# Kernel optimization log

Measured on AMD Instinct MI355X. Metric: run time of the kernel, lower is better.

## Reference

```python
import math
import jax, jax.numpy as jnp
import numpy as np

EMBED = 1024
INTERNAL = 1024  # EMBED // downsample_rate(=1)
HEADS = 16


def setup_inputs() -> dict:
    key = jax.random.key(0)
    ks = jax.random.split(key, 11)
    b, n, m = 2, 2048, 2048
    s = 1.0 / math.sqrt(EMBED)
    inp = {
        "q": jax.random.normal(ks[0], (b, n, EMBED), jnp.float32),
        "k": jax.random.normal(ks[1], (b, m, EMBED), jnp.float32),
        "v": jax.random.normal(ks[2], (b, m, EMBED), jnp.float32),
        # Linear params (torch Linear: y = x @ W.T + b); store as [in, out].
        "Wq": jax.random.normal(ks[3], (EMBED, INTERNAL), jnp.float32) * s,
        "bq": jax.random.normal(ks[4], (INTERNAL,), jnp.float32) * s,
        "Wk": jax.random.normal(ks[5], (EMBED, INTERNAL), jnp.float32) * s,
        "bk": jax.random.normal(ks[6], (INTERNAL,), jnp.float32) * s,
        "Wv": jax.random.normal(ks[7], (EMBED, INTERNAL), jnp.float32) * s,
        "bv": jax.random.normal(ks[8], (INTERNAL,), jnp.float32) * s,
        "Wo": jax.random.normal(ks[9], (INTERNAL, EMBED), jnp.float32) * s,
        "bo": jax.random.normal(ks[10], (EMBED,), jnp.float32) * s,
    }
    return inp


def _split_heads(x):  # [b, n, c] -> [b, h, n, c/h]
    b, n, c = x.shape
    return x.reshape(b, n, HEADS, c // HEADS).transpose(0, 2, 1, 3)


def reference(q, k, v, Wq, bq, Wk, bk, Wv, bv, Wo, bo):
    qh = _split_heads(q @ Wq + bq)
    kh = _split_heads(k @ Wk + bk)
    vh = _split_heads(v @ Wv + bv)
    c_per_head = kh.shape[-1]
    attn = jnp.einsum("bhnc,bhmc->bhnm", qh, kh) / math.sqrt(c_per_head)
    attn = jax.nn.softmax(attn, axis=-1)
    out = jnp.einsum("bhnm,bhmc->bhnc", attn, vh)
    b, h, n, ch = out.shape
    out = out.transpose(0, 2, 1, 3).reshape(b, n, h * ch)
    return out @ Wo + bo
```

## Files before the change

kernel.cpp:

```cpp
#include <hip/hip_runtime.h>

#define EMBED 1024
#define HEADS 16
#define DHEAD 64
#define BATCH 2
#define SEQ 2048
#define ROWS (BATCH*SEQ)
#define SZA (ROWS*EMBED)
#define SW (EMBED*EMBED)

typedef _Float16 f16;
typedef __attribute__((ext_vector_type(2))) __fp16 h16x2;
typedef __attribute__((ext_vector_type(4))) _Float16 f16x4;
typedef __attribute__((ext_vector_type(8))) _Float16 f16x8;
typedef __attribute__((ext_vector_type(4))) float f32x4;

__device__ __forceinline__ void gld16(const f16* g, f16* lds) {
  __builtin_amdgcn_global_load_lds(
      (const __attribute__((address_space(1))) void*)g,
      (__attribute__((address_space(3))) void*)lds, 16, 0, 0);
}

__global__ __launch_bounds__(256) void pre_kernel(
    const float* __restrict__ q, const float* __restrict__ k,
    const float* __restrict__ v, f16* __restrict__ qc,
    f16* __restrict__ kc, f16* __restrict__ vc,
    const float* __restrict__ w0, const float* __restrict__ w1,
    const float* __restrict__ w2, const float* __restrict__ w3,
    f16* __restrict__ o0, f16* __restrict__ o1,
    f16* __restrict__ o2, f16* __restrict__ o3) {
  __shared__ float tile[32][33];
  const int y = blockIdx.y;
  if (y < 3) {
    const float* in = y == 0 ? q : y == 1 ? k : v;
    f16* out       = y == 0 ? qc : y == 1 ? kc : vc;
    int i = blockIdx.x * 256 + threadIdx.x;
    float4 f = ((const float4* __restrict__)in)[i];
    union { f16 h[4]; short4 s4; } u;
    u.h[0] = (f16)f.x; u.h[1] = (f16)f.y; u.h[2] = (f16)f.z; u.h[3] = (f16)f.w;
    ((short4* __restrict__)out)[i] = u.s4;
    return;
  }
  const int x = blockIdx.x;
  const int z = x >> 10, by = (x >> 5) & 31, bx = x & 31;
  const float* in = z == 0 ? w0 : z == 1 ? w1 : z == 2 ? w2 : w3;
  f16* out       = z == 0 ? o0 : z == 1 ? o1 : z == 2 ? o2 : o3;
  int tx = threadIdx.x & 31, ty = threadIdx.x >> 5;
  #pragma unroll
  for (int i = 0; i < 32; i += 8)
    tile[ty + i][tx] = in[(by*32 + ty + i)*EMBED + bx*32 + tx];
  __syncthreads();
  #pragma unroll
  for (int i = 0; i < 32; i += 8)
    out[(bx*32 + ty + i)*EMBED + by*32 + tx] = (f16)tile[tx][ty + i];
}

__global__ __launch_bounds__(256) void gemm3_kernel(
    const f16* __restrict__ qc, const f16* __restrict__ kc, const f16* __restrict__ vc,
    const f16* __restrict__ Wqt, const f16* __restrict__ Wkt, const f16* __restrict__ Wvt,
    const float* __restrict__ bq, const float* __restrict__ bk, const float* __restrict__ bv,
    f16* __restrict__ Qp, f16* __restrict__ Kp, f16* __restrict__ Vtg) {
  __shared__ __align__(16) f16 As[128*32];
  __shared__ __align__(16) f16 Bs[128*32];
  const int z = blockIdx.y;
  const f16 *A, *Bt; const float* bias; f16* C;
  int mbase, nbase, N, biasrow;
  if (z == 0)      { A=qc;  Bt=Wqt; bias=bq; C=Qp;  mbase=(blockIdx.x&31)*128; nbase=(blockIdx.x>>5)*128; N=EMBED; biasrow=0; }
  else if (z == 1) { A=kc;  Bt=Wkt; bias=bk; C=Kp;  mbase=(blockIdx.x&31)*128; nbase=(blockIdx.x>>5)*128; N=EMBED; biasrow=0; }
  else             { A=Wvt; Bt=vc;  bias=bv; C=Vtg; mbase=(blockIdx.x&7)*128;  nbase=(blockIdx.x>>3)*128; N=ROWS;  biasrow=1; }
  const int K = EMBED;
  const int tid = threadIdx.x;
  const int wave = tid >> 6, lane = tid & 63;
  const int lg = lane >> 4, lr = lane & 15;
  const int wm = (wave >> 1) * 64, wn = (wave & 1) * 64;
  const int sr = lane >> 2, sc = (lane & 3) * 8;
  const f16* gA0 = A  + (size_t)(mbase + wave*16 + sr)*K + sc;
  const f16* gA1 = A  + (size_t)(mbase + 64 + wave*16 + sr)*K + sc;
  const f16* gB0 = Bt + (size_t)(nbase + wave*16 + sr)*K + sc;
  const f16* gB1 = Bt + (size_t)(nbase + 64 + wave*16 + sr)*K + sc;
  f16* lA0 = &As[(wave*16)*32];
  f16* lA1 = &As[(64 + wave*16)*32];
  f16* lB0 = &Bs[(wave*16)*32];
  f16* lB1 = &Bs[(64 + wave*16)*32];
  f32x4 acc[4][4] = {};
  for (int k0 = 0; k0 < K; k0 += 32) {
    __syncthreads();
    gld16(gA0 + k0, lA0);
    gld16(gA1 + k0, lA1);
    gld16(gB0 + k0, lB0);
    gld16(gB1 + k0, lB1);
    __syncthreads();
    f16x8 af[4], bf[4];
    #pragma unroll
    for (int mt = 0; mt < 4; mt++)
      af[mt] = *(const f16x8*)&As[(wm + mt*16 + lr)*32 + lg*8];
    #pragma unroll
    for (int nt = 0; nt < 4; nt++)
      bf[nt] = *(const f16x8*)&Bs[(wn + nt*16 + lr)*32 + lg*8];
    #pragma unroll
    for (int mt = 0; mt < 4; mt++)
      #pragma unroll
      for (int nt = 0; nt < 4; nt++)
        acc[mt][nt] = __builtin_amdgcn_mfma_f32_16x16x32_f16(af[mt], bf[nt], acc[mt][nt], 0, 0, 0);
  }
  #pragma unroll
  for (int mt = 0; mt < 4; mt++)
    #pragma unroll
    for (int nt = 0; nt < 4; nt++)
      #pragma unroll
      for (int i = 0; i < 4; i++) {
        int row = mbase + wm + mt*16 + lg*4 + i;
        int col = nbase + wn + nt*16 + lr;
        float val = acc[mt][nt][i] + (biasrow ? bias[row] : bias[col]);
        C[(size_t)row*N + col] = (f16)val;
      }
}

__global__ __launch_bounds__(256) void gemmo_kernel(
    const f16* __restrict__ A, const f16* __restrict__ Bt,
    const float* __restrict__ bias, float* __restrict__ Cf) {
  __shared__ __align__(16) f16 As[128*32];
  __shared__ __align__(16) f16 Bs[64*32];
  const int K = EMBED, N = EMBED;
  const int tid = threadIdx.x;
  const int wave = tid >> 6, lane = tid & 63;
  const int lg = lane >> 4, lr = lane & 15;
  const int mbase = blockIdx.x * 128, nbase = blockIdx.y * 64;
  const int wm = (wave >> 1) * 64, wn = (wave & 1) * 32;
  const int sr = wave*16 + (lane >> 2), sc = (lane & 3) * 8;
  const f16* gA0 = A  + (size_t)(mbase + sr)*K + sc;
  const f16* gA1 = A  + (size_t)(mbase + 64 + sr)*K + sc;
  const f16* gB  = Bt + (size_t)(nbase + sr)*K + sc;
  f16* lA0 = &As[(wave*16)*32];
  f16* lA1 = &As[(64 + wave*16)*32];
  f16* lB  = &Bs[(wave*16)*32];
  f32x4 acc[4][2] = {};
  for (int k0 = 0; k0 < K; k0 += 32) {
    __syncthreads();
    gld16(gA0 + k0, lA0);
    gld16(gA1 + k0, lA1);
    gld16(gB  + k0, lB);
    __syncthreads();
    f16x8 af[4], bf[2];
    #pragma unroll
    for (int mt = 0; mt < 4; mt++)
      af[mt] = *(const f16x8*)&As[(wm + mt*16 + lr)*32 + lg*8];
    #pragma unroll
    for (int nt = 0; nt < 2; nt++)
      bf[nt] = *(const f16x8*)&Bs[(wn + nt*16 + lr)*32 + lg*8];
    #pragma unroll
    for (int mt = 0; mt < 4; mt++)
      #pragma unroll
      for (int nt = 0; nt < 2; nt++)
        acc[mt][nt] = __builtin_amdgcn_mfma_f32_16x16x32_f16(af[mt], bf[nt], acc[mt][nt], 0, 0, 0);
  }
  #pragma unroll
  for (int mt = 0; mt < 4; mt++)
    #pragma unroll
    for (int nt = 0; nt < 2; nt++)
      #pragma unroll
      for (int i = 0; i < 4; i++) {
        int row = mbase + wm + mt*16 + lg*4 + i;
        int col = nbase + wn + nt*16 + lr;
        Cf[(size_t)row*N + col] = acc[mt][nt][i] + bias[col];
      }
}

__global__ __launch_bounds__(256, 2) void attn_kernel(
    const f16* __restrict__ Qp, const f16* __restrict__ Kp,
    const f16* __restrict__ Vt, f16* __restrict__ Ob) {
  __shared__ __align__(16) f16 Ks[4096];
  __shared__ __align__(16) f16 Vs[4096];
  const int tid = threadIdx.x;
  const int wave = tid >> 6, lane = tid & 63;
  const int lg = lane >> 4, lr = lane & 15;
  const int gid = blockIdx.x;
  const int bh  = (gid & 7)*4 + ((gid >> 3) & 3);
  const int qblk = gid >> 5;
  const int h = bh & 15, b = bh >> 4;
  const int q0 = qblk*128 + wave*32;
  const f16* Qh = Qp + (size_t)b*SEQ*EMBED + h*DHEAD;
  const f16* Kh = Kp + (size_t)b*SEQ*EMBED + h*DHEAD;
  const f16* Vh = Vt + (size_t)h*DHEAD*ROWS + (size_t)b*SEQ;

  const f16* kst[2]; const f16* vst[2]; f16* kdst[2]; f16* vdst[2];
  #pragma unroll
  for (int m = 0; m < 2; m++) {
    int sgrp = m*4 + wave;
    int srow = sgrp*8 + (lane >> 3);
    int sch  = (lane & 7) ^ (srow & 7);
    int prow = ((srow>>5)&1)*32 + ((srow>>4)&1)*4 + ((srow>>2)&3)*8 + (srow&3);
    kst[m] = Kh + (size_t)prow*EMBED + sch*8;
    vst[m] = Vh + (size_t)srow*ROWS + sch*8;
    kdst[m] = &Ks[sgrp*512];
    vdst[m] = &Vs[sgrp*512];
  }

  f16x8 qf[2][2];
  #pragma unroll
  for (int qb = 0; qb < 2; qb++)
    #pragma unroll
    for (int ds = 0; ds < 2; ds++)
      qf[qb][ds] = *(const f16x8*)&Qh[(size_t)(q0 + qb*16 + lr)*EMBED + ds*32 + lg*8];

  const int c0 = ((lg)     ^ (lr & 7)) * 8;
  const int c1 = ((4 + lg) ^ (lr & 7)) * 8;

  f32x4 o[4][2] = {};
  float ls[2] = {};
  const float SC = 0.18033688011f;

  for (int kt = 0; kt < SEQ; kt += 64) {
    __syncthreads();
    gld16(kst[0] + (size_t)kt*EMBED, kdst[0]);
    gld16(kst[1] + (size_t)kt*EMBED, kdst[1]);
    gld16(vst[0] + kt, vdst[0]);
    gld16(vst[1] + kt, vdst[1]);
    __syncthreads();

    f16x8 ka[4][2];
    #pragma unroll
    for (int nb = 0; nb < 4; nb++) {
      ka[nb][0] = *(const f16x8*)&Ks[(nb*16 + lr)*64 + c0];
      ka[nb][1] = *(const f16x8*)&Ks[(nb*16 + lr)*64 + c1];
    }
    f32x4 sa[2][4];
    #pragma unroll
    for (int nb = 0; nb < 4; nb++)
      #pragma unroll
      for (int qb = 0; qb < 2; qb++) {
        f32x4 z = {0.f, 0.f, 0.f, 0.f};
        z = __builtin_amdgcn_mfma_f32_16x16x32_f16(ka[nb][0], qf[qb][0], z, 0, 0, 0);
        z = __builtin_amdgcn_mfma_f32_16x16x32_f16(ka[nb][1], qf[qb][1], z, 0, 0, 0);
        sa[qb][nb] = z;
      }

    f16x8 va[4][2];
    #pragma unroll
    for (int dm = 0; dm < 4; dm++) {
      va[dm][0] = *(const f16x8*)&Vs[(dm*16 + lr)*64 + c0];
      va[dm][1] = *(const f16x8*)&Vs[(dm*16 + lr)*64 + c1];
    }

    f16x8 pf[2][2];
    #pragma unroll
    for (int qb = 0; qb < 2; qb++) {
      float p[4][4];
      #pragma unroll
      for (int nb = 0; nb < 4; nb++)
        #pragma unroll
        for (int i = 0; i < 4; i++) {
          p[nb][i] = __builtin_amdgcn_exp2f(sa[qb][nb][i]*SC - 8.0f);
          ls[qb] += p[nb][i];
        }
      union { f16x8 v; h16x2 h2[4]; } u0, u1;
      u0.h2[0] = __builtin_amdgcn_cvt_pkrtz(p[0][0], p[0][1]);
      u0.h2[1] = __builtin_amdgcn_cvt_pkrtz(p[0][2], p[0][3]);
      u0.h2[2] = __builtin_amdgcn_cvt_pkrtz(p[1][0], p[1][1]);
      u0.h2[3] = __builtin_amdgcn_cvt_pkrtz(p[1][2], p[1][3]);
      u1.h2[0] = __builtin_amdgcn_cvt_pkrtz(p[2][0], p[2][1]);
      u1.h2[1] = __builtin_amdgcn_cvt_pkrtz(p[2][2], p[2][3]);
      u1.h2[2] = __builtin_amdgcn_cvt_pkrtz(p[3][0], p[3][1]);
      u1.h2[3] = __builtin_amdgcn_cvt_pkrtz(p[3][2], p[3][3]);
      pf[qb][0] = u0.v;
      pf[qb][1] = u1.v;
    }

    #pragma unroll
    for (int ks = 0; ks < 2; ks++)
      #pragma unroll
      for (int qb = 0; qb < 2; qb++)
        #pragma unroll
        for (int dm = 0; dm < 4; dm++)
          o[dm][qb] = __builtin_amdgcn_mfma_f32_16x16x32_f16(va[dm][ks], pf[qb][ks], o[dm][qb], 0, 0, 0);
  }

  float inv[2];
  #pragma unroll
  for (int qb = 0; qb < 2; qb++) {
    float s = ls[qb];
    s += __shfl_xor(s, 16);
    s += __shfl_xor(s, 32);
    inv[qb] = 1.f / s;
  }

  #pragma unroll
  for (int qb = 0; qb < 2; qb++) {
    const size_t rowb = (size_t)(b*SEQ + q0 + qb*16 + lr)*EMBED + h*DHEAD;
    #pragma unroll
    for (int dm = 0; dm < 4; dm++) {
      f16x4 w;
      #pragma unroll
      for (int i = 0; i < 4; i++) w[i] = (f16)(o[dm][qb][i] * inv[qb]);
      *(f16x4*)&Ob[rowb + dm*16 + 4*lg] = w;
    }
  }
}

extern "C" void kernel_launch(void* const* d_in, const int* in_sizes, int n_in,
                              void* d_out, int out_size, void* d_ws, size_t ws_size,
                              hipStream_t stream) {
  (void)in_sizes; (void)n_in; (void)out_size; (void)ws_size;
  const float* q  = (const float*)d_in[0];
  const float* k  = (const float*)d_in[1];
  const float* v  = (const float*)d_in[2];
  const float* Wq = (const float*)d_in[3];
  const float* bq = (const float*)d_in[4];
  const float* Wk = (const float*)d_in[5];
  const float* bk = (const float*)d_in[6];
  const float* Wv = (const float*)d_in[7];
  const float* bv = (const float*)d_in[8];
  const float* Wo = (const float*)d_in[9];
  const float* bo = (const float*)d_in[10];
  float* out = (float*)d_out;

  f16* w   = (f16*)d_ws;
  f16* qc  = w;
  f16* kc  = qc + SZA;
  f16* vc  = kc + SZA;
  f16* Qp  = vc + SZA;
  f16* Kp  = Qp + SZA;
  f16* Vtg = Kp + SZA;
  f16* Ob  = Vtg + SZA;
  f16* Wqt = Ob + SZA;
  f16* Wkt = Wqt + SW;
  f16* Wvt = Wkt + SW;
  f16* Wot = Wvt + SW;

  dim3 pg(4096, 4);
  pre_kernel<<<pg, 256, 0, stream>>>(q, k, v, qc, kc, vc,
                                     Wq, Wk, Wv, Wo, Wqt, Wkt, Wvt, Wot);
  dim3 g3(256, 3);
  gemm3_kernel<<<g3, 256, 0, stream>>>(qc, kc, vc, Wqt, Wkt, Wvt, bq, bk, bv, Qp, Kp, Vtg);
  attn_kernel<<<512, 256, 0, stream>>>(Qp, Kp, Vtg, Ob);
  dim3 go(ROWS/128, EMBED/64);
  gemmo_kernel<<<go, 256, 0, stream>>>(Ob, Wot, bo, out);
}
```

Baseline: 216.4 us.

## Double-buffer K/V tiles and fold softmax scale and row sums into MFMA

The attention loop now uses double-buffered LDS for K and V. The next tile's global-to-LDS loads are issued before computing on the current tile, and only one barrier remains per iteration. The softmax scale is applied in the Q projection epilogue (z==0), and the -8 offset becomes the MFMA accumulator init, which removes per-element FMAs. Row sums are computed by an extra MFMA against a ones vector instead of scalar adds and shuffles. s_setprio brackets are added around the MFMA sections. LDS use doubles, which may reduce occupancy, and the extra MFMAs add matrix-core work.

```diff
diff --git a/kernel.cpp b/kernel.cpp
--- a/kernel.cpp
+++ b/kernel.cpp
@@ -112,6 +112,7 @@
         int row = mbase + wm + mt*16 + lg*4 + i;
         int col = nbase + wn + nt*16 + lr;
         float val = acc[mt][nt][i] + (biasrow ? bias[row] : bias[col]);
+        if (z == 0) val *= 0.18033688011f;
         C[(size_t)row*N + col] = (f16)val;
       }
 }
@@ -169,8 +170,8 @@
 __global__ __launch_bounds__(256, 2) void attn_kernel(
     const f16* __restrict__ Qp, const f16* __restrict__ Kp,
     const f16* __restrict__ Vt, f16* __restrict__ Ob) {
-  __shared__ __align__(16) f16 Ks[4096];
-  __shared__ __align__(16) f16 Vs[4096];
+  __shared__ __align__(16) f16 Ks[2*4096];
+  __shared__ __align__(16) f16 Vs[2*4096];
   const int tid = threadIdx.x;
   const int wave = tid >> 6, lane = tid & 63;
   const int lg = lane >> 4, lr = lane & 15;
@@ -207,39 +208,52 @@
   const int c1 = ((4 + lg) ^ (lr & 7)) * 8;
 
   f32x4 o[4][2] = {};
-  float ls[2] = {};
-  const float SC = 0.18033688011f;
-
-  for (int kt = 0; kt < SEQ; kt += 64) {
-    __syncthreads();
-    gld16(kst[0] + (size_t)kt*EMBED, kdst[0]);
-    gld16(kst[1] + (size_t)kt*EMBED, kdst[1]);
-    gld16(vst[0] + kt, vdst[0]);
-    gld16(vst[1] + kt, vdst[1]);
-    __syncthreads();
+  f32x4 lacc[2] = {};
+  const f32x4 NEG8 = {-8.f, -8.f, -8.f, -8.f};
+  f16x8 onesf;
+  #pragma unroll
+  for (int i = 0; i < 8; i++) onesf[i] = (f16)1.0f;
+
+  gld16(kst[0], kdst[0]);
+  gld16(kst[1], kdst[1]);
+  gld16(vst[0], vdst[0]);
+  gld16(vst[1], vdst[1]);
+  __syncthreads();
+
+  #pragma unroll 2
+  for (int t = 0; t < 32; ++t) {
+    const int bo = (t & 1) * 4096;
+    if (t < 31) {
+      const int po = 4096 - bo;
+      const size_t kt = (size_t)(t + 1) * 64;
+      gld16(kst[0] + kt*EMBED, kdst[0] + po);
+      gld16(kst[1] + kt*EMBED, kdst[1] + po);
+      gld16(vst[0] + kt, vdst[0] + po);
+      gld16(vst[1] + kt, vdst[1] + po);
+    }
 
     f16x8 ka[4][2];
     #pragma unroll
     for (int nb = 0; nb < 4; nb++) {
-      ka[nb][0] = *(const f16x8*)&Ks[(nb*16 + lr)*64 + c0];
-      ka[nb][1] = *(const f16x8*)&Ks[(nb*16 + lr)*64 + c1];
+      ka[nb][0] = *(const f16x8*)&Ks[bo + (nb*16 + lr)*64 + c0];
+      ka[nb][1] = *(const f16x8*)&Ks[bo + (nb*16 + lr)*64 + c1];
     }
     f32x4 sa[2][4];
+    __builtin_amdgcn_s_setprio(1);
     #pragma unroll
     for (int nb = 0; nb < 4; nb++)
       #pragma unroll
       for (int qb = 0; qb < 2; qb++) {
-        f32x4 z = {0.f, 0.f, 0.f, 0.f};
-        z = __builtin_amdgcn_mfma_f32_16x16x32_f16(ka[nb][0], qf[qb][0], z, 0, 0, 0);
-        z = __builtin_amdgcn_mfma_f32_16x16x32_f16(ka[nb][1], qf[qb][1], z, 0, 0, 0);
-        sa[qb][nb] = z;
+        f32x4 z = __builtin_amdgcn_mfma_f32_16x16x32_f16(ka[nb][0], qf[qb][0], NEG8, 0, 0, 0);
+        sa[qb][nb] = __builtin_amdgcn_mfma_f32_16x16x32_f16(ka[nb][1], qf[qb][1], z, 0, 0, 0);
       }
+    __builtin_amdgcn_s_setprio(0);
 
     f16x8 va[4][2];
     #pragma unroll
     for (int dm = 0; dm < 4; dm++) {
-      va[dm][0] = *(const f16x8*)&Vs[(dm*16 + lr)*64 + c0];
-      va[dm][1] = *(const f16x8*)&Vs[(dm*16 + lr)*64 + c1];
+      va[dm][0] = *(const f16x8*)&Vs[bo + (dm*16 + lr)*64 + c0];
+      va[dm][1] = *(const f16x8*)&Vs[bo + (dm*16 + lr)*64 + c1];
     }
 
     f16x8 pf[2][2];
@@ -249,10 +263,8 @@
       #pragma unroll
       for (int nb = 0; nb < 4; nb++)
         #pragma unroll
-        for (int i = 0; i < 4; i++) {
-          p[nb][i] = __builtin_amdgcn_exp2f(sa[qb][nb][i]*SC - 8.0f);
-          ls[qb] += p[nb][i];
-        }
+        for (int i = 0; i < 4; i++)
+          p[nb][i] = __builtin_amdgcn_exp2f(sa[qb][nb][i]);
       union { f16x8 v; h16x2 h2[4]; } u0, u1;
       u0.h2[0] = __builtin_amdgcn_cvt_pkrtz(p[0][0], p[0][1]);
       u0.h2[1] = __builtin_amdgcn_cvt_pkrtz(p[0][2], p[0][3]);
@@ -266,23 +278,22 @@
       pf[qb][1] = u1.v;
     }
 
+    __builtin_amdgcn_s_setprio(1);
     #pragma unroll
     for (int ks = 0; ks < 2; ks++)
       #pragma unroll
-      for (int qb = 0; qb < 2; qb++)
+      for (int qb = 0; qb < 2; qb++) {
         #pragma unroll
         for (int dm = 0; dm < 4; dm++)
           o[dm][qb] = __builtin_amdgcn_mfma_f32_16x16x32_f16(va[dm][ks], pf[qb][ks], o[dm][qb], 0, 0, 0);
-  }
-
-  float inv[2];
-  #pragma unroll
-  for (int qb = 0; qb < 2; qb++) {
-    float s = ls[qb];
-    s += __shfl_xor(s, 16);
-    s += __shfl_xor(s, 32);
-    inv[qb] = 1.f / s;
-  }
+        lacc[qb] = __builtin_amdgcn_mfma_f32_16x16x32_f16(onesf, pf[qb][ks], lacc[qb], 0, 0, 0);
+      }
+    __builtin_amdgcn_s_setprio(0);
+
+    __syncthreads();
+  }
+
+  const float inv[2] = { 1.f / lacc[0][0], 1.f / lacc[1][0] };
 
   #pragma unroll
   for (int qb = 0; qb < 2; qb++) {
```

New measurement: 207.1 us. 4.3% less time.
